# Kernel optimization log

Measured on AMD Instinct MI355X. Metric: run time of the kernel, lower is better.

Reference implementation:

```python
import jax, jax.numpy as jnp
import numpy as np

IN_C = 256
OUT_C = 256
K_NUM = 6
EDGE_TYPE = 3


def setup_inputs() -> dict:
    key = jax.random.key(0)
    k1, k2, k3, k4, k5 = jax.random.split(key, 5)
    N, T, V = 32, 64, 25
    x = jax.random.normal(k1, (N, IN_C, T, V), dtype=jnp.float32)
    A = jax.random.uniform(k2, (K_NUM - EDGE_TYPE, V, V), dtype=jnp.float32)
    B = jax.random.uniform(k3, (N, EDGE_TYPE, V, V), dtype=jnp.float32)
    lamda_act = jnp.float32(0.5)
    # ConvTranspose2d with kernel (1,1), stride 1, no padding == pointwise matmul.
    # torch weight shape (in, out, 1, 1) -> store squeezed (in, out).
    W = jax.random.normal(k4, (IN_C, OUT_C * K_NUM), dtype=jnp.float32) * (1.0 / np.sqrt(IN_C))
    b = jax.random.normal(k5, (OUT_C * K_NUM,), dtype=jnp.float32) * 0.01
    return {"x": x, "A": A, "B": B, "lamda_act": lamda_act, "W": W, "b": b}


def reference(x, A, B, lamda_act, W, b):
    # pointwise transposed conv (1x1 kernel) -> channel matmul
    y = jnp.einsum('nctv,co->notv', x, W) + b[None, :, None, None]  # [N, K*C_out, T, V]
    n, kc, t, v = y.shape
    y = y.reshape(n, K_NUM, kc // K_NUM, t, v)
    x1 = jnp.einsum('nkctv,kvw->nctw', y[:, :K_NUM - EDGE_TYPE], A)
    x2 = jnp.einsum('nkctv,nkvw->nctw', y[:, K_NUM - EDGE_TYPE:], B)
    x_sum = x1 + x2 * lamda_act
    return (x_sum, A)
```

## Files before the change

### kernel.cpp

```cpp
#include <hip/hip_runtime.h>
#include <hip/hip_bf16.h>
#include <stdint.h>

typedef __bf16 bf16_t;
typedef bf16_t bf16x8 __attribute__((ext_vector_type(8)));
typedef float f32x4 __attribute__((ext_vector_type(4)));

#define DEVI static __device__ __forceinline__

constexpr int NB = 32, CIN = 256, COUT = 256, KNUM = 6, ET = 3, TDIM = 64, VV = 25;
constexpr int KD   = KNUM * CIN;
constexpr long OUT0 = (long)NB * COUT * TDIM * VV;
constexpr int ACNT = ET * VV * VV;

constexpr int NSTEP = 24;
constexpr int WP3_CHUNKS = NSTEP * 2048;
constexpr size_t WP3_BYTES  = (size_t)WP3_CHUNKS * 16;
constexpr size_t BIAS_OFF   = WP3_BYTES;
constexpr size_t BIAS_BYTES = (size_t)NB * VV * COUT * 4;
constexpr size_t WS_NEED    = BIAS_OFF + BIAS_BYTES;

DEVI unsigned packbf(float lo, float hi) {
  unsigned short a = __builtin_bit_cast(unsigned short, (bf16_t)lo);
  unsigned short b = __builtin_bit_cast(unsigned short, (bf16_t)hi);
  return ((unsigned)b << 16) | (unsigned)a;
}

__global__ __launch_bounds__(256) void prep_kernel(
    const float* __restrict__ A, const float* __restrict__ Bm,
    const float* __restrict__ lam_p, const float* __restrict__ W,
    const float* __restrict__ bvec, bf16_t* __restrict__ wp3,
    float* __restrict__ biasmat, float* __restrict__ outA)
{
  int idx = blockIdx.x * 256 + threadIdx.x;
  constexpr int S1 = WP3_CHUNKS;
  constexpr int S2 = S1 + NB * VV * COUT;
  constexpr int S3 = S2 + ACNT;
  if (idx < S1) {
    int s  = idx >> 11;
    int r  = idx & 2047;
    int mi = r >> 7;
    int kk = (r >> 6) & 1;
    int ln = r & 63;
    int lg = ln >> 4, lw = ln & 15;
    int cb = s / 6, k = s - cb * 6;
    int cibase = cb * 64 + (lg + 4 * kk) * 8;
    int col = (k << 8) + mi * 16 + lw;
    bf16_t* dst = wp3 + ((long)idx << 3);
    #pragma unroll
    for (int e = 0; e < 8; ++e)
      dst[e] = (bf16_t)W[(cibase + e) * KD + col];
  } else if (idx < S2) {
    int j = idx - S1;
    int c = j & 255;
    int nw = j >> 8;
    int w = nw % VV;
    int n = nw / VV;
    float lam = lam_p[0];
    float s = 0.f;
    for (int k = 0; k < KNUM; ++k) {
      float sk = 0.f;
      if (k < ET) {
        for (int v = 0; v < VV; ++v) sk += A[(k * VV + v) * VV + w];
      } else {
        for (int v = 0; v < VV; ++v) sk += Bm[(((n * ET) + (k - ET)) * VV + v) * VV + w];
        sk *= lam;
      }
      s += bvec[(k << 8) + c] * sk;
    }
    biasmat[j] = s;
  } else if (idx < S3) {
    int j = idx - S2;
    outA[j] = A[j];
  }
}

__global__ __launch_bounds__(512, 4) void fused_kernel(
    const float* __restrict__ x, const float* __restrict__ A,
    const float* __restrict__ Bm, const float* __restrict__ lam_p,
    const bf16_t* __restrict__ wp3, const float* __restrict__ biasmat,
    float* __restrict__ out)
{
  __shared__ __align__(16) bf16_t Bs[2 * 128 * 64];
  __shared__ __align__(16) bf16_t Xs[256 * 32];
  __shared__ __align__(16) bf16_t Ms[KNUM * 32 * 32];

  const int b = blockIdx.x;
  const int n = b >> 4;
  const int t0 = (b & 15) << 2;
  const int tid = threadIdx.x;
  const int wv = tid >> 6, ln = tid & 63;
  const int lw = ln & 15, lg = ln >> 4;
  const float lam = lam_p[0];

  for (int i = tid; i < KNUM * 32 * 32; i += 512) {
    int R = i >> 5, v = i & 31;
    int k = i >> 10, w = (i >> 5) & 31;
    float val = 0.f;
    if (w < VV && v < VV)
      val = (k < ET) ? A[(k * VV + v) * VV + w]
                     : lam * Bm[(((n * ET) + (k - ET)) * VV + v) * VV + w];
    int sw2 = (w & 3) ^ ((w >> 2) & 3);
    int byteoff = R * 64 + ((((v >> 3) ^ sw2) & 3) << 4) + ((v & 7) << 1);
    *(bf16_t*)((char*)Ms + byteoff) = (bf16_t)val;
  }

  f32x4 acc[4][4] = {};
  const int m_base = (wv >> 1) * 64;
  const int mb4 = (wv >> 1) * 4;
  const int n_base = (wv & 1) * 64;
  const f32x4 z4 = {0.f, 0.f, 0.f, 0.f};
  const int msw2 = (lw & 3) ^ ((lw >> 2) & 3);

  #pragma unroll 1
  for (int cb = 0; cb < 4; ++cb) {
    __syncthreads();
    if (tid < 256) {
      int ci = tid >> 2, dt = tid & 3;
      const float* xp = x + ((long)(n * CIN + cb * 64 + ci) * TDIM + t0 + dt) * VV;
      float xv[25];
      #pragma unroll
      for (int v = 0; v < VV; ++v) xv[v] = xp[v];
      int row = dt * 64 + ci;
      int sw = (row & 3) ^ ((row >> 2) & 3);
      #pragma unroll
      for (int g = 0; g < 4; ++g) {
        char* base = (char*)Xs + row * 64 + ((g ^ sw) & 3) * 16;
        #pragma unroll
        for (int p = 0; p < 4; ++p) {
          int v0 = g * 8 + p * 2;
          float lo = (v0     < VV) ? xv[v0 < VV ? v0 : 0]     : 0.f;
          float hi = (v0 + 1 < VV) ? xv[v0 + 1 < VV ? v0 + 1 : 0] : 0.f;
          *(unsigned*)(base + p * 4) = packbf(lo, hi);
        }
      }
    }
    __syncthreads();

    #pragma unroll 1
    for (int k = 0; k < KNUM; ++k) {
      const int s = cb * 6 + k;
      const int buf = (s & 1) * (128 * 64);
      const bf16_t* wpS = wp3 + (((long)s * 2048 + (long)mb4 * 128 + ln) << 3);

      bf16x8 mb0 = *(const bf16x8*)((const char*)Ms + (k * 32 + lw) * 64 + (((lg ^ msw2) & 3) << 4));
      bf16x8 mb1 = *(const bf16x8*)((const char*)Ms + (k * 32 + 16 + lw) * 64 + (((lg ^ msw2) & 3) << 4));
      #pragma unroll
      for (int rt = 0; rt < 2; ++rt) {
        int arow = wv * 32 + rt * 16 + lw;
        int sw = (arow & 3) ^ ((arow >> 2) & 3);
        int off = ((lg ^ sw) & 3) << 4;
        bf16x8 af = *(const bf16x8*)((const char*)Xs + arow * 64 + off);
        f32x4 d0 = __builtin_amdgcn_mfma_f32_16x16x32_bf16(af, mb0, z4, 0, 0, 0);
        f32x4 d1 = __builtin_amdgcn_mfma_f32_16x16x32_bf16(af, mb1, z4, 0, 0, 0);
        int rbase = wv * 32 + rt * 16 + (lg << 2);
        int dt = rbase >> 6, ci0 = rbase & 63;
        int r0 = dt * 32 + lw;
        int g0 = ((ci0 >> 3) ^ (r0 & 7)) & 7;
        char* c0 = (char*)(Bs + buf) + r0 * 128 + (g0 << 4) + ((ci0 << 1) & 15);
        *(unsigned*)(c0)     = packbf(d0[0], d0[1]);
        *(unsigned*)(c0 + 4) = packbf(d0[2], d0[3]);
        char* c1 = (char*)(Bs + buf) + (r0 + 16) * 128 + (g0 << 4) + ((ci0 << 1) & 15);
        *(unsigned*)(c1)     = packbf(d1[0], d1[1]);
        *(unsigned*)(c1 + 4) = packbf(d1[2], d1[3]);
      }
      __syncthreads();

      __builtin_amdgcn_s_setprio(1);
      {
        bf16x8 af2a[4];
        #pragma unroll
        for (int i = 0; i < 4; ++i)
          af2a[i] = *(const bf16x8*)(wpS + ((i * 128) << 3));
        bf16x8 bf2[4];
        #pragma unroll
        for (int j = 0; j < 4; ++j) {
          int rr = n_base + j * 16 + lw;
          int gg = (lg ^ (rr & 7)) & 7;
          bf2[j] = *(const bf16x8*)((const char*)(Bs + buf) + rr * 128 + (gg << 4));
        }
        #pragma unroll
        for (int i = 0; i < 4; ++i)
          #pragma unroll
          for (int j = 0; j < 4; ++j)
            acc[i][j] = __builtin_amdgcn_mfma_f32_16x16x32_bf16(af2a[i], bf2[j], acc[i][j], 0, 0, 0);
      }
      {
        bf16x8 af2b[4];
        #pragma unroll
        for (int i = 0; i < 4; ++i)
          af2b[i] = *(const bf16x8*)(wpS + ((i * 128 + 64) << 3));
        bf16x8 bf2[4];
        #pragma unroll
        for (int j = 0; j < 4; ++j) {
          int rr = n_base + j * 16 + lw;
          int gg = ((4 + lg) ^ (rr & 7)) & 7;
          bf2[j] = *(const bf16x8*)((const char*)(Bs + buf) + rr * 128 + (gg << 4));
        }
        #pragma unroll
        for (int i = 0; i < 4; ++i)
          #pragma unroll
          for (int j = 0; j < 4; ++j)
            acc[i][j] = __builtin_amdgcn_mfma_f32_16x16x32_bf16(af2b[i], bf2[j], acc[i][j], 0, 0, 0);
      }
      __builtin_amdgcn_s_setprio(0);
      __syncthreads();
    }
  }

  #pragma unroll
  for (int j = 0; j < 4; ++j) {
    int colb = n_base + j * 16 + lw;
    int dt = colb >> 5, w = colb & 31;
    if (w < VV) {
      float* ob = out + (long)n * 409600 + (t0 + dt) * 25 + w;
      const float* brow = biasmat + (n * 25 + w) * 256;
      #pragma unroll
      for (int i = 0; i < 4; ++i) {
        int mb = m_base + i * 16 + (lg << 2);
        #pragma unroll
        for (int r = 0; r < 4; ++r) {
          int m = mb + r;
          ob[(long)m * 1600] = acc[i][j][r] + brow[m];
        }
      }
    }
  }
}

__global__ __launch_bounds__(256) void fallback_kernel(
    const float* __restrict__ x, const float* __restrict__ A,
    const float* __restrict__ Bm, const float* __restrict__ lam_p,
    const float* __restrict__ W, const float* __restrict__ bvec,
    float* __restrict__ out)
{
  __shared__ __align__(16) float xs[CIN][28];
  __shared__ __align__(16) float Ms[KNUM][VV][28];
  const int nt = blockIdx.x;
  const int n = nt >> 6, t = nt & 63;
  const int tid = threadIdx.x;
  const float lam = lam_p[0];

  const float* xp = x + (((long)(n * CIN + tid) * TDIM + t) * VV);
  #pragma unroll
  for (int v = 0; v < VV; ++v) xs[tid][v] = xp[v];
  xs[tid][25] = xs[tid][26] = xs[tid][27] = 0.f;
  for (int i = tid; i < KNUM * VV * VV; i += 256) {
    int k = i / (VV * VV);
    int r = i - k * VV * VV;
    int v = r / VV;
    int w = r - v * VV;
    Ms[k][v][w] = (k < ET) ? A[(k * VV + v) * VV + w]
                           : lam * Bm[(((n * ET) + (k - ET)) * VV + v) * VV + w];
    if (w == 24) { Ms[k][v][25] = Ms[k][v][26] = Ms[k][v][27] = 0.f; }
  }
  __syncthreads();

  float oacc[28] = {};
  for (int k = 0; k < KNUM; ++k) {
    float yv[28];
    float bv = bvec[(k << 8) + tid];
    #pragma unroll
    for (int v = 0; v < 28; ++v) yv[v] = 0.f;
    for (int ci = 0; ci < CIN; ++ci) {
      float wl = W[ci * KD + (k << 8) + tid];
      const f32x4* x4 = (const f32x4*)&xs[ci][0];
      #pragma unroll
      for (int q = 0; q < 7; ++q) {
        f32x4 xv = x4[q];
        yv[q*4+0] += wl*xv[0]; yv[q*4+1] += wl*xv[1];
        yv[q*4+2] += wl*xv[2]; yv[q*4+3] += wl*xv[3];
      }
    }
    #pragma unroll
    for (int v = 0; v < VV; ++v) {
      float yvv = yv[v] + bv;
      const f32x4* m4 = (const f32x4*)&Ms[k][v][0];
      #pragma unroll
      for (int q = 0; q < 7; ++q) {
        f32x4 mv = m4[q];
        oacc[q*4+0] += yvv*mv[0]; oacc[q*4+1] += yvv*mv[1];
        oacc[q*4+2] += yvv*mv[2]; oacc[q*4+3] += yvv*mv[3];
      }
    }
  }
  float* op = out + (((long)(n * COUT + tid) * TDIM + t) * VV);
  #pragma unroll
  for (int w = 0; w < VV; ++w) op[w] = oacc[w];
}

__global__ void copyA_kernel(const float* __restrict__ A, float* __restrict__ outA) {
  int i = blockIdx.x * 256 + threadIdx.x;
  if (i < ACNT) outA[i] = A[i];
}

extern "C" void kernel_launch(void* const* d_in, const int* in_sizes, int n_in,
                              void* d_out, int out_size, void* d_ws, size_t ws_size,
                              hipStream_t stream) {
  const float* x   = (const float*)d_in[0];
  const float* A   = (const float*)d_in[1];
  const float* Bm  = (const float*)d_in[2];
  const float* lam = (const float*)d_in[3];
  const float* W   = (const float*)d_in[4];
  const float* bv  = (const float*)d_in[5];
  float* out = (float*)d_out;

  if (d_ws != nullptr && ws_size >= WS_NEED) {
    bf16_t* wp3     = (bf16_t*)d_ws;
    float*  biasmat = (float*)((char*)d_ws + BIAS_OFF);
    constexpr int PREP_ITEMS = WP3_CHUNKS + NB * VV * COUT + ACNT;
    prep_kernel<<<(PREP_ITEMS + 255) / 256, 256, 0, stream>>>(A, Bm, lam, W, bv, wp3, biasmat, out + OUT0);
    fused_kernel<<<NB * 16, 512, 0, stream>>>(x, A, Bm, lam, wp3, biasmat, out);
  } else {
    fallback_kernel<<<NB * TDIM, 256, 0, stream>>>(x, A, Bm, lam, W, bv, out);
    copyA_kernel<<<(ACNT + 255) / 256, 256, 0, stream>>>(A, out + OUT0);
  }
}
```

Baseline: 85.26 us.

## Stage epilogue through LDS for vectorized stores, pad LDS rows, hoist weight loads

The output epilogue now writes accumulators plus bias into shared memory one 64-channel slice at a time, then emits coalesced 16-byte global stores of the contiguous 100-float (4 timesteps × 25 joints) runs. This replaces scattered 4-byte stores that had a 1600-float stride. Xs and Ms rows are padded from 64 to 80 bytes to cut LDS bank conflicts. The first batch of global weight fragment loads is hoisted ahead of the stage-1 MFMA, and the per-iteration trailing barrier is removed. The epilogue adds four serialized rounds of barriers and raises LDS usage, which may affect occupancy.

```diff
diff --git a/kernel.cpp b/kernel.cpp
--- a/kernel.cpp
+++ b/kernel.cpp
@@ -82,8 +82,8 @@
     float* __restrict__ out)
 {
   __shared__ __align__(16) bf16_t Bs[2 * 128 * 64];
-  __shared__ __align__(16) bf16_t Xs[256 * 32];
-  __shared__ __align__(16) bf16_t Ms[KNUM * 32 * 32];
+  __shared__ __align__(16) bf16_t Xs[256 * 40];
+  __shared__ __align__(16) bf16_t Ms[KNUM * 32 * 40];
 
   const int b = blockIdx.x;
   const int n = b >> 4;
@@ -101,7 +101,7 @@
       val = (k < ET) ? A[(k * VV + v) * VV + w]
                      : lam * Bm[(((n * ET) + (k - ET)) * VV + v) * VV + w];
     int sw2 = (w & 3) ^ ((w >> 2) & 3);
-    int byteoff = R * 64 + ((((v >> 3) ^ sw2) & 3) << 4) + ((v & 7) << 1);
+    int byteoff = R * 80 + ((((v >> 3) ^ sw2) & 3) << 4) + ((v & 7) << 1);
     *(bf16_t*)((char*)Ms + byteoff) = (bf16_t)val;
   }
 
@@ -125,7 +125,7 @@
       int sw = (row & 3) ^ ((row >> 2) & 3);
       #pragma unroll
       for (int g = 0; g < 4; ++g) {
-        char* base = (char*)Xs + row * 64 + ((g ^ sw) & 3) * 16;
+        char* base = (char*)Xs + row * 80 + ((g ^ sw) & 3) * 16;
         #pragma unroll
         for (int p = 0; p < 4; ++p) {
           int v0 = g * 8 + p * 2;
@@ -143,14 +143,19 @@
       const int buf = (s & 1) * (128 * 64);
       const bf16_t* wpS = wp3 + (((long)s * 2048 + (long)mb4 * 128 + ln) << 3);
 
-      bf16x8 mb0 = *(const bf16x8*)((const char*)Ms + (k * 32 + lw) * 64 + (((lg ^ msw2) & 3) << 4));
-      bf16x8 mb1 = *(const bf16x8*)((const char*)Ms + (k * 32 + 16 + lw) * 64 + (((lg ^ msw2) & 3) << 4));
+      bf16x8 af2a[4];
+      #pragma unroll
+      for (int i = 0; i < 4; ++i)
+        af2a[i] = *(const bf16x8*)(wpS + ((i * 128) << 3));
+
+      bf16x8 mb0 = *(const bf16x8*)((const char*)Ms + (k * 32 + lw) * 80 + (((lg ^ msw2) & 3) << 4));
+      bf16x8 mb1 = *(const bf16x8*)((const char*)Ms + (k * 32 + 16 + lw) * 80 + (((lg ^ msw2) & 3) << 4));
       #pragma unroll
       for (int rt = 0; rt < 2; ++rt) {
         int arow = wv * 32 + rt * 16 + lw;
         int sw = (arow & 3) ^ ((arow >> 2) & 3);
         int off = ((lg ^ sw) & 3) << 4;
-        bf16x8 af = *(const bf16x8*)((const char*)Xs + arow * 64 + off);
+        bf16x8 af = *(const bf16x8*)((const char*)Xs + arow * 80 + off);
         f32x4 d0 = __builtin_amdgcn_mfma_f32_16x16x32_bf16(af, mb0, z4, 0, 0, 0);
         f32x4 d1 = __builtin_amdgcn_mfma_f32_16x16x32_bf16(af, mb1, z4, 0, 0, 0);
         int rbase = wv * 32 + rt * 16 + (lg << 2);
@@ -168,10 +173,6 @@
 
       __builtin_amdgcn_s_setprio(1);
       {
-        bf16x8 af2a[4];
-        #pragma unroll
-        for (int i = 0; i < 4; ++i)
-          af2a[i] = *(const bf16x8*)(wpS + ((i * 128) << 3));
         bf16x8 bf2[4];
         #pragma unroll
         for (int j = 0; j < 4; ++j) {
@@ -204,27 +205,43 @@
             acc[i][j] = __builtin_amdgcn_mfma_f32_16x16x32_bf16(af2b[i], bf2[j], acc[i][j], 0, 0, 0);
       }
       __builtin_amdgcn_s_setprio(0);
-      __syncthreads();
-    }
-  }
-
-  #pragma unroll
-  for (int j = 0; j < 4; ++j) {
-    int colb = n_base + j * 16 + lw;
-    int dt = colb >> 5, w = colb & 31;
-    if (w < VV) {
-      float* ob = out + (long)n * 409600 + (t0 + dt) * 25 + w;
-      const float* brow = biasmat + (n * 25 + w) * 256;
-      #pragma unroll
-      for (int i = 0; i < 4; ++i) {
-        int mb = m_base + i * 16 + (lg << 2);
-        #pragma unroll
-        for (int r = 0; r < 4; ++r) {
-          int m = mb + r;
-          ob[(long)m * 1600] = acc[i][j][r] + brow[m];
+    }
+  }
+
+  __syncthreads();
+  float* eb = (float*)Bs;
+  #pragma unroll 1
+  for (int rnd = 0; rnd < 4; ++rnd) {
+    if ((wv >> 1) == rnd) {
+      #pragma unroll
+      for (int j = 0; j < 4; ++j) {
+        int col = n_base + j * 16 + lw;
+        int dt = col >> 5, w = col & 31;
+        if (w < VV) {
+          const float* brow = biasmat + (n * 25 + w) * 256 + rnd * 64;
+          #pragma unroll
+          for (int i = 0; i < 4; ++i) {
+            #pragma unroll
+            for (int r = 0; r < 4; ++r) {
+              int cl = i * 16 + (lg << 2) + r;
+              eb[cl * 100 + dt * 25 + w] = acc[i][j][r] + brow[cl];
+            }
+          }
         }
       }
     }
+    __syncthreads();
+    #pragma unroll
+    for (int it = 0; it < 4; ++it) {
+      int idx = it * 512 + tid;
+      if (idx < 1600) {
+        int cl = idx / 25, f4 = idx - cl * 25;
+        f32x4 val = *(const f32x4*)(eb + cl * 100 + f4 * 4);
+        *(f32x4*)(out + (long)n * 409600 + (long)(rnd * 64 + cl) * 1600
+                      + t0 * 25 + f4 * 4) = val;
+      }
+    }
+    __syncthreads();
   }
 }
 
```

Measured after the change: 74.02 us. 1.15x faster.
